# Optimization experiments

Measured on AMD Instinct MI355X. Metric: run time of the kernel, lower is better.

The kernel has to match this reference:

```python
import jax, jax.numpy as jnp
import numpy as np

NEG_SLOPE = 0.2


def _add_self_loops(edge_index, n_nodes):
    loops = jnp.arange(n_nodes, dtype=edge_index.dtype)
    src = jnp.concatenate([edge_index[0], loops])
    dst = jnp.concatenate([edge_index[1], loops])
    return src, dst


def gat_conv(x, src, dst, W, a_src, a_dst, b, n_nodes):
    # h: [N, F] transformed node features
    h = x @ W
    # per-node attention logits, then gather per-edge
    s_n = h @ a_src  # [N]
    d_n = h @ a_dst  # [N]
    e = jax.nn.leaky_relu(s_n[src] + d_n[dst], NEG_SLOPE)  # [E]
    # softmax over incoming edges of each destination node (self-loops guarantee >=1 edge per node)
    m = jax.ops.segment_max(e, dst, num_segments=n_nodes)  # [N]
    p = jnp.exp(e - m[dst])
    denom = jax.ops.segment_sum(p, dst, num_segments=n_nodes)  # [N]
    alpha = p / denom[dst]  # [E]
    # scatter weighted source features to destinations
    out = jax.ops.segment_sum(alpha[:, None] * h[src], dst, num_segments=n_nodes)
    return out + b


def setup_inputs() -> dict:
    key = jax.random.key(0)
    ks = jax.random.split(key, 11)
    N, E, D = 50000, 800000, 128
    x = jax.random.normal(ks[0], (N, D), dtype=jnp.float32)
    edge_index = jax.random.randint(ks[1], (2, E), 0, N, dtype=jnp.int64)
    p = lambda k, shape: jax.random.normal(k, shape, dtype=jnp.float32) * 0.05
    return {
        "x": x,
        "edge_index": edge_index,
        "W1": p(ks[2], (D, D)), "a_src1": p(ks[3], (D,)), "a_dst1": p(ks[4], (D,)), "b1": p(ks[5], (D,)),
        "W2": p(ks[6], (D, D)), "a_src2": p(ks[7], (D,)), "a_dst2": p(ks[8], (D,)), "b2": p(ks[9], (D,)),
    }


def reference(x, edge_index, W1, a_src1, a_dst1, b1, W2, a_src2, a_dst2, b2):
    n_nodes = x.shape[0]
    src, dst = _add_self_loops(edge_index, n_nodes)
    h = jax.nn.relu(gat_conv(x, src, dst, W1, a_src1, a_dst1, b1, n_nodes))
    h = gat_conv(h, src, dst, W2, a_src2, a_dst2, b2, n_nodes)
    return h.mean(axis=0)  # [out_dim]
```

## Files before the change

### kernel.cpp

```cpp
#include <hip/hip_runtime.h>
#include <hip/hip_fp8.h>
#include <math.h>

#define NEG_SLOPE 0.2f
#define D 128
#define SCAN_NB 128
#define NBLK_BIN 256
#define NPB 128
#define LOG_NPB 7

typedef unsigned int uint;
typedef unsigned short ushort;
typedef unsigned char uchar;
typedef short bf16x8 __attribute__((ext_vector_type(8)));
typedef float f32x4 __attribute__((ext_vector_type(4)));

__device__ __forceinline__ float bflo(uint u) { return __uint_as_float(u << 16); }
__device__ __forceinline__ float bfhi(uint u) { return __uint_as_float(u & 0xffff0000u); }
__device__ __forceinline__ uint packbf(float lo, float hi) {
    uint a = __float_as_uint(lo), b = __float_as_uint(hi);
    uint ra = (a + 0x7fffu + ((a >> 16) & 1u)) >> 16;
    uint rb = (b + 0x7fffu + ((b >> 16) & 1u)) >> 16;
    return ra | (rb << 16);
}
__device__ __forceinline__ ushort bf16_1(float f) {
    uint a = __float_as_uint(f);
    return (ushort)((a + 0x7fffu + ((a >> 16) & 1u)) >> 16);
}
__device__ __forceinline__ uint relu_pk(uint u) {
    uint lo = (u & 0x00008000u) ? 0u : (u & 0x0000ffffu);
    uint hi = (u & 0x80000000u) ? 0u : (u & 0xffff0000u);
    return lo | hi;
}

__device__ __forceinline__ float fp8tof(uint b) {
    __hip_fp8_e4m3 v; v.__x = (__hip_fp8_storage_t)b; return (float)v;
}
__device__ __forceinline__ uchar ftofp8(float f) {
    __hip_fp8_e4m3 v(f); return (uchar)v.__x;
}

union U4B { uint4 u; bf16x8 h; };


__global__ __launch_bounds__(256) void bin_hist(const int* __restrict__ dst,
                                                int E, int M, int nbuck,
                                                int* __restrict__ hist) {
    extern __shared__ int lh[];
    for (int k = threadIdx.x; k < nbuck; k += 256) lh[k] = 0;
    __syncthreads();
    int chunk = (M + gridDim.x - 1) / gridDim.x;
    int e0 = blockIdx.x * chunk;
    int e1 = e0 + chunk; if (e1 > M) e1 = M;
    for (int e = e0 + threadIdx.x; e < e1; e += 256) {
        int d = (e < E) ? dst[e] : (e - E);
        atomicAdd(&lh[d >> LOG_NPB], 1);
    }
    __syncthreads();
    for (int k = threadIdx.x; k < nbuck; k += 256)
        hist[(size_t)k * NBLK_BIN + blockIdx.x] = lh[k];
}

__global__ __launch_bounds__(256) void scan_pass1(const int* __restrict__ cnt, int n,
                                                  int* __restrict__ bsum) {
    int chunk = (n + SCAN_NB - 1) / SCAN_NB;
    int b0 = blockIdx.x * chunk;
    int b1 = b0 + chunk; if (b1 > n) b1 = n;
    int s = 0;
    for (int i = b0 + threadIdx.x; i < b1; i += 256) s += cnt[i];
    for (int off = 32; off; off >>= 1) s += __shfl_xor(s, off);
    __shared__ int ws[4];
    int lane = threadIdx.x & 63, wave = threadIdx.x >> 6;
    if (lane == 0) ws[wave] = s;
    __syncthreads();
    if (threadIdx.x == 0) bsum[blockIdx.x] = ws[0] + ws[1] + ws[2] + ws[3];
}

__global__ __launch_bounds__(128) void scan_pass2(int* __restrict__ bsum) {
    int t = threadIdx.x;
    int v = bsum[t];
    int lane = t & 63, wave = t >> 6;
    int x = v;
#pragma unroll
    for (int off = 1; off < 64; off <<= 1) {
        int y = __shfl_up(x, off);
        if (lane >= off) x += y;
    }
    __shared__ int wtot[2];
    if (lane == 63) wtot[wave] = x;
    __syncthreads();
    int base = (wave == 1) ? wtot[0] : 0;
    bsum[t] = base + x - v;
}

__global__ __launch_bounds__(256) void scan_pass3(const int* __restrict__ cnt, int n,
                                                  const int* __restrict__ bsum,
                                                  int* __restrict__ outp, int total) {
    int chunk = (n + SCAN_NB - 1) / SCAN_NB;
    int b0 = blockIdx.x * chunk;
    int b1 = b0 + chunk; if (b1 > n) b1 = n;
    int tchunk = (chunk + 255) / 256;
    int t0 = b0 + threadIdx.x * tchunk;
    int t1 = t0 + tchunk; if (t1 > b1) t1 = b1;
    int s = 0;
    for (int i = t0; i < t1; ++i) s += cnt[i];
    int lane = threadIdx.x & 63, wave = threadIdx.x >> 6;
    int x = s;
#pragma unroll
    for (int off = 1; off < 64; off <<= 1) {
        int y = __shfl_up(x, off);
        if (lane >= off) x += y;
    }
    __shared__ int wtot[4];
    if (lane == 63) wtot[wave] = x;
    __syncthreads();
    int wbase = 0;
    for (int w = 0; w < wave; ++w) wbase += wtot[w];
    int run = bsum[blockIdx.x] + wbase + x - s;
    for (int i = t0; i < t1; ++i) {
        outp[i] = run;
        run += cnt[i];
    }
    if (blockIdx.x == 0 && threadIdx.x == 0) outp[n] = total;
}

__global__ __launch_bounds__(256) void bin_scatter(const int* __restrict__ esrc,
                                                   const int* __restrict__ dst,
                                                   int E, int M, int nbuck,
                                                   const int* __restrict__ hist_off,
                                                   int* __restrict__ packed) {
    extern __shared__ int cur[];
    for (int k = threadIdx.x; k < nbuck; k += 256)
        cur[k] = hist_off[(size_t)k * NBLK_BIN + blockIdx.x];
    __syncthreads();
    int chunk = (M + gridDim.x - 1) / gridDim.x;
    int e0 = blockIdx.x * chunk;
    int e1 = e0 + chunk; if (e1 > M) e1 = M;
    for (int e = e0 + threadIdx.x; e < e1; e += 256) {
        int d, s;
        if (e < E) { d = dst[e]; s = esrc[e]; }
        else       { d = e - E;  s = d; }
        int k = d >> LOG_NPB;
        int pos = atomicAdd(&cur[k], 1);
        packed[pos] = ((d & (NPB - 1)) << 16) | s;
    }
}

__global__ __launch_bounds__(256) void bucket_sort(const int* __restrict__ packed,
                                                   const int* __restrict__ hist_off,
                                                   int N, int M,
                                                   int* __restrict__ row_ptr,
                                                   int* __restrict__ csr_src) {
    __shared__ int lcnt[NPB];
    __shared__ int lcur[NPB];
    __shared__ int wtot2[2];
    int t = threadIdx.x;
    int node0 = blockIdx.x << LOG_NPB;
    int nlocal = N - node0; if (nlocal > NPB) nlocal = NPB;
    int base = hist_off[(size_t)blockIdx.x * NBLK_BIN];
    int bend = hist_off[(size_t)(blockIdx.x + 1) * NBLK_BIN];

    if (t < NPB) lcnt[t] = 0;
    __syncthreads();
    for (int j = base + t; j < bend; j += 256)
        atomicAdd(&lcnt[packed[j] >> 16], 1);
    __syncthreads();

    int v = (t < NPB) ? lcnt[t] : 0;
    int lane = t & 63, wv = t >> 6;
    int x = v;
#pragma unroll
    for (int off = 1; off < 64; off <<= 1) {
        int y = __shfl_up(x, off);
        if (lane >= off) x += y;
    }
    if (t < NPB && lane == 63) wtot2[wv] = x;
    __syncthreads();
    if (t < NPB) {
        int bw = (wv == 1) ? wtot2[0] : 0;
        int ex = bw + x - v;
        lcur[t] = ex;
        if (t < nlocal) row_ptr[node0 + t] = base + ex;
    }
    if (blockIdx.x == 0 && t == 0) row_ptr[N] = M;
    __syncthreads();

    for (int j = base + t; j < bend; j += 256) {
        int p = packed[j];
        int dl = p >> 16;
        int pos = atomicAdd(&lcur[dl], 1);
        csr_src[base + pos] = p & 0xffff;
    }
}

__global__ __launch_bounds__(128) void wt_kernel2(const float* __restrict__ W1,
                                                  const float* __restrict__ W2,
                                                  ushort* __restrict__ Wt1,
                                                  ushort* __restrict__ Wt2) {
    int col = blockIdx.x & 127;
    const float* W = (blockIdx.x < 128) ? W1 : W2;
    ushort* Wt = (blockIdx.x < 128) ? Wt1 : Wt2;
    Wt[(size_t)col * D + threadIdx.x] = bf16_1(W[(size_t)threadIdx.x * D + col]);
}

template <bool RELU_IN, bool BF16_IN>
__global__ __launch_bounds__(256) void gemm_mfma(const void* __restrict__ Xv,
                                                 const ushort* __restrict__ Wt,
                                                 const float* __restrict__ a_src,
                                                 const float* __restrict__ a_dst,
                                                 uchar* __restrict__ H,
                                                 float* __restrict__ s_n,
                                                 float* __restrict__ d_n, int n) {
    __shared__ float sred[2][32][5];
    int wave = threadIdx.x >> 6;
    int lane = threadIdx.x & 63;
    int row0 = blockIdx.x * 32;
    int kgrp = (lane >> 4) * 8;

    bf16x8 afrag[2][4];
#pragma unroll
    for (int rh = 0; rh < 2; ++rh) {
        int arow = row0 + rh * 16 + (lane & 15);
        bool rvalid = arow < n;
        if (BF16_IN) {
            const ushort* X = (const ushort*)Xv;
            const ushort* xp = X + (size_t)arow * D + kgrp;
#pragma unroll
            for (int kk = 0; kk < 4; ++kk) {
                U4B u; u.u = make_uint4(0, 0, 0, 0);
                if (rvalid) {
                    u.u = *(const uint4*)(xp + kk * 32);
                    if (RELU_IN) {
                        u.u.x = relu_pk(u.u.x); u.u.y = relu_pk(u.u.y);
                        u.u.z = relu_pk(u.u.z); u.u.w = relu_pk(u.u.w);
                    }
                }
                afrag[rh][kk] = u.h;
            }
        } else {
            const float* X = (const float*)Xv;
            const float* xp = X + (size_t)arow * D + kgrp;
#pragma unroll
            for (int kk = 0; kk < 4; ++kk) {
                U4B u; u.u = make_uint4(0, 0, 0, 0);
                if (rvalid) {
                    float4 v0 = *(const float4*)(xp + kk * 32);
                    float4 v1 = *(const float4*)(xp + kk * 32 + 4);
                    if (RELU_IN) {
                        v0.x = fmaxf(v0.x, 0.f); v0.y = fmaxf(v0.y, 0.f);
                        v0.z = fmaxf(v0.z, 0.f); v0.w = fmaxf(v0.w, 0.f);
                        v1.x = fmaxf(v1.x, 0.f); v1.y = fmaxf(v1.y, 0.f);
                        v1.z = fmaxf(v1.z, 0.f); v1.w = fmaxf(v1.w, 0.f);
                    }
                    u.u.x = packbf(v0.x, v0.y); u.u.y = packbf(v0.z, v0.w);
                    u.u.z = packbf(v1.x, v1.y); u.u.w = packbf(v1.z, v1.w);
                }
                afrag[rh][kk] = u.h;
            }
        }
    }

    bf16x8 bfrag[2][4];
#pragma unroll
    for (int t = 0; t < 2; ++t) {
        int bcol = wave * 32 + t * 16 + (lane & 15);
        const ushort* wp = Wt + (size_t)bcol * D + kgrp;
#pragma unroll
        for (int kk = 0; kk < 4; ++kk) {
            U4B u; u.u = *(const uint4*)(wp + kk * 32);
            bfrag[t][kk] = u.h;
        }
    }

    f32x4 acc[2][2];
#pragma unroll
    for (int rh = 0; rh < 2; ++rh)
#pragma unroll
        for (int t = 0; t < 2; ++t) acc[rh][t] = (f32x4){0.f, 0.f, 0.f, 0.f};

#pragma unroll
    for (int kk = 0; kk < 4; ++kk) {
#pragma unroll
        for (int rh = 0; rh < 2; ++rh) {
#pragma unroll
            for (int t = 0; t < 2; ++t) {
                acc[rh][t] = __builtin_amdgcn_mfma_f32_16x16x32_bf16(
                    afrag[rh][kk], bfrag[t][kk], acc[rh][t], 0, 0, 0);
            }
        }
    }

    int ccol = wave * 32 + (lane & 15);
    float as0 = a_src[ccol], as1 = a_src[ccol + 16];
    float ad0 = a_dst[ccol], ad1 = a_dst[ccol + 16];
#pragma unroll
    for (int rh = 0; rh < 2; ++rh) {
        int crow0 = row0 + rh * 16 + (lane >> 4) * 4;
#pragma unroll
        for (int i = 0; i < 4; ++i) {
            int r = crow0 + i;
            if (r < n) {
                H[(size_t)r * D + ccol]      = ftofp8(acc[rh][0][i]);
                H[(size_t)r * D + ccol + 16] = ftofp8(acc[rh][1][i]);
            }
            float ps = acc[rh][0][i] * as0 + acc[rh][1][i] * as1;
            float pd = acc[rh][0][i] * ad0 + acc[rh][1][i] * ad1;
#pragma unroll
            for (int off = 1; off < 16; off <<= 1) {
                ps += __shfl_xor(ps, off);
                pd += __shfl_xor(pd, off);
            }
            if ((lane & 15) == 0) {
                int rl = rh * 16 + (lane >> 4) * 4 + i;
                sred[0][rl][wave] = ps;
                sred[1][rl][wave] = pd;
            }
        }
    }
    __syncthreads();
    if (threadIdx.x < 64) {
        int which = threadIdx.x >> 5;
        int rl = threadIdx.x & 31;
        float v = sred[which][rl][0] + sred[which][rl][1] +
                  sred[which][rl][2] + sred[which][rl][3];
        int r = row0 + rl;
        if (r < n) { if (which) d_n[r] = v; else s_n[r] = v; }
    }
}

__global__ __launch_bounds__(256) void gat_aggregate(const uchar* __restrict__ H,
                                                     const float* __restrict__ s_n,
                                                     const float* __restrict__ d_n,
                                                     const int* __restrict__ row_ptr,
                                                     const int* __restrict__ csr_src,
                                                     const float* __restrict__ bias,
                                                     ushort* __restrict__ OUT, int n) {
    __shared__ float lp[4][64];
    __shared__ int   ls[4][64];
    int wave = threadIdx.x >> 6;
    int lane = threadIdx.x & 63;
    int node = blockIdx.x * 4 + wave;
    bool valid = node < n;

    int beg = 0, end = 0;
    float dn = 0.f;
    if (valid) {
        beg = row_ptr[node];
        end = row_ptr[node + 1];
        dn  = d_n[node];
    }
    int deg = end - beg;
    bool small = (deg <= 64);

    int g  = lane >> 4;
    int gl = lane & 15;
    int c0 = gl * 8;

    float p = 0.f;
    int   sidx = 0;
    float inv = 1.0f;

    if (small) {
        float e = -INFINITY;
        if (lane < deg) {
            sidx = csr_src[beg + lane];
            float t = s_n[sidx] + dn;
            e = t > 0.f ? t : NEG_SLOPE * t;
        }
        float m = e;
        for (int off = 32; off; off >>= 1) m = fmaxf(m, __shfl_xor(m, off));
        p = (lane < deg) ? __expf(e - m) : 0.f;
        float sum = p;
        for (int off = 32; off; off >>= 1) sum += __shfl_xor(sum, off);
        inv = 1.0f / sum;
    }
    lp[wave][lane] = p;
    ls[wave][lane] = sidx;
    __syncthreads();
    if (!valid) return;

    float acc[8] = {0.f, 0.f, 0.f, 0.f, 0.f, 0.f, 0.f, 0.f};

    if (small) {
        for (int j = g; j < deg; j += 4) {
            int   sv = ls[wave][j];
            float al = lp[wave][j];
            uint2 hv = *(const uint2*)(H + (size_t)sv * D + c0);
            acc[0] = fmaf(al, fp8tof(hv.x & 0xff), acc[0]);
            acc[1] = fmaf(al, fp8tof((hv.x >> 8) & 0xff), acc[1]);
            acc[2] = fmaf(al, fp8tof((hv.x >> 16) & 0xff), acc[2]);
            acc[3] = fmaf(al, fp8tof(hv.x >> 24), acc[3]);
            acc[4] = fmaf(al, fp8tof(hv.y & 0xff), acc[4]);
            acc[5] = fmaf(al, fp8tof((hv.y >> 8) & 0xff), acc[5]);
            acc[6] = fmaf(al, fp8tof((hv.y >> 16) & 0xff), acc[6]);
            acc[7] = fmaf(al, fp8tof(hv.y >> 24), acc[7]);
        }
    } else {
        float m = -INFINITY;
        for (int j = beg + lane; j < end; j += 64) {
            float t = s_n[csr_src[j]] + dn;
            t = t > 0.f ? t : NEG_SLOPE * t;
            m = fmaxf(m, t);
        }
        for (int off = 32; off; off >>= 1) m = fmaxf(m, __shfl_xor(m, off));
        float sum = 0.f;
        for (int j = beg + lane; j < end; j += 64) {
            float t = s_n[csr_src[j]] + dn;
            t = t > 0.f ? t : NEG_SLOPE * t;
            sum += __expf(t - m);
        }
        for (int off = 32; off; off >>= 1) sum += __shfl_xor(sum, off);
        inv = 1.0f / sum;

        for (int j = beg + g; j < end; j += 4) {
            int s = csr_src[j];
            float t = s_n[s] + dn;
            t = t > 0.f ? t : NEG_SLOPE * t;
            float alpha = __expf(t - m);
            uint2 hv = *(const uint2*)(H + (size_t)s * D + c0);
            acc[0] = fmaf(alpha, fp8tof(hv.x & 0xff), acc[0]);
            acc[1] = fmaf(alpha, fp8tof((hv.x >> 8) & 0xff), acc[1]);
            acc[2] = fmaf(alpha, fp8tof((hv.x >> 16) & 0xff), acc[2]);
            acc[3] = fmaf(alpha, fp8tof(hv.x >> 24), acc[3]);
            acc[4] = fmaf(alpha, fp8tof(hv.y & 0xff), acc[4]);
            acc[5] = fmaf(alpha, fp8tof((hv.y >> 8) & 0xff), acc[5]);
            acc[6] = fmaf(alpha, fp8tof((hv.y >> 16) & 0xff), acc[6]);
            acc[7] = fmaf(alpha, fp8tof(hv.y >> 24), acc[7]);
        }
    }

#pragma unroll
    for (int i = 0; i < 8; ++i) {
        acc[i] += __shfl_xor(acc[i], 16);
        acc[i] += __shfl_xor(acc[i], 32);
    }
    if (g == 0) {
        float4 b0 = *(const float4*)(bias + c0);
        float4 b1 = *(const float4*)(bias + c0 + 4);
        uint4 o;
        o.x = packbf(acc[0] * inv + b0.x, acc[1] * inv + b0.y);
        o.y = packbf(acc[2] * inv + b0.z, acc[3] * inv + b0.w);
        o.z = packbf(acc[4] * inv + b1.x, acc[5] * inv + b1.y);
        o.w = packbf(acc[6] * inv + b1.z, acc[7] * inv + b1.w);
        *(uint4*)(OUT + (size_t)node * D + c0) = o;
    }
}


__global__ void zero_out(float* __restrict__ out) { out[threadIdx.x] = 0.f; }

__global__ __launch_bounds__(256) void mean_reduce(const ushort* __restrict__ X, int n,
                                                   float* __restrict__ out) {
    __shared__ float sacc[16][128];
    int rg = threadIdx.x >> 4;
    int ft = threadIdx.x & 15;
    int c0 = ft * 8;
    float a[8] = {0.f, 0.f, 0.f, 0.f, 0.f, 0.f, 0.f, 0.f};
    int stride = gridDim.x * 16;
    for (int r = blockIdx.x * 16 + rg; r < n; r += stride) {
        uint4 v = *(const uint4*)(X + (size_t)r * D + c0);
        a[0] += bflo(v.x); a[1] += bfhi(v.x);
        a[2] += bflo(v.y); a[3] += bfhi(v.y);
        a[4] += bflo(v.z); a[5] += bfhi(v.z);
        a[6] += bflo(v.w); a[7] += bfhi(v.w);
    }
#pragma unroll
    for (int j = 0; j < 8; ++j) sacc[rg][c0 + j] = a[j];
    __syncthreads();
    if (threadIdx.x < 128) {
        float s = 0.f;
#pragma unroll
        for (int g = 0; g < 16; ++g) s += sacc[g][threadIdx.x];
        atomicAdd(&out[threadIdx.x], s * (1.0f / (float)n));
    }
}


extern "C" void kernel_launch(void* const* d_in, const int* in_sizes, int n_in,
                              void* d_out, int out_size, void* d_ws, size_t ws_size,
                              hipStream_t stream) {
    const float* x      = (const float*)d_in[0];
    const int*   ei     = (const int*)d_in[1];
    const float* W1     = (const float*)d_in[2];
    const float* a_src1 = (const float*)d_in[3];
    const float* a_dst1 = (const float*)d_in[4];
    const float* b1     = (const float*)d_in[5];
    const float* W2     = (const float*)d_in[6];
    const float* a_src2 = (const float*)d_in[7];
    const float* a_dst2 = (const float*)d_in[8];
    const float* b2     = (const float*)d_in[9];
    float* out = (float*)d_out;

    int N = in_sizes[0] / D;
    int E = in_sizes[1] / 2;
    const int* esrc = ei;
    const int* edst = ei + E;
    int M = E + N;
    int NBUCK = (N + NPB - 1) >> LOG_NPB;
    int NHIST = NBUCK * NBLK_BIN;
    size_t smem = (size_t)NBUCK * 4;

    char* p = (char*)d_ws;
    auto alloc = [&](size_t bytes) -> void* {
        void* r = (void*)p;
        p += (bytes + 511) & ~(size_t)511;
        return r;
    };
    int*    hist     = (int*)alloc((size_t)NHIST * 4);
    int*    hist_off = (int*)alloc((size_t)(NHIST + 1) * 4);
    int*    packed   = (int*)alloc((size_t)M * 4);
    int*    csr_src  = (int*)alloc((size_t)M * 4);
    int*    row_ptr  = (int*)alloc((size_t)(N + 1) * 4);
    int*    bsum     = (int*)alloc((size_t)SCAN_NB * 4);
    uchar*  h        = (uchar*)alloc((size_t)N * D);
    ushort* io       = (ushort*)alloc((size_t)N * D * 2);
    float*  s_n      = (float*)alloc((size_t)N * 4);
    float*  d_n      = (float*)alloc((size_t)N * 4);
    ushort* wt1      = (ushort*)alloc((size_t)D * D * 2);
    ushort* wt2      = (ushort*)alloc((size_t)D * D * 2);

    bin_hist<<<NBLK_BIN, 256, smem, stream>>>(edst, E, M, NBUCK, hist);
    scan_pass1<<<SCAN_NB, 256, 0, stream>>>(hist, NHIST, bsum);
    scan_pass2<<<1, 128, 0, stream>>>(bsum);
    scan_pass3<<<SCAN_NB, 256, 0, stream>>>(hist, NHIST, bsum, hist_off, M);
    bin_scatter<<<NBLK_BIN, 256, smem, stream>>>(esrc, edst, E, M, NBUCK, hist_off, packed);
    bucket_sort<<<NBUCK, 256, 0, stream>>>(packed, hist_off, N, M, row_ptr, csr_src);

    wt_kernel2<<<256, 128, 0, stream>>>(W1, W2, wt1, wt2);

    gemm_mfma<false, false><<<(N + 31) / 32, 256, 0, stream>>>(x, wt1, a_src1, a_dst1, h, s_n, d_n, N);
    gat_aggregate<<<(N + 3) / 4, 256, 0, stream>>>(h, s_n, d_n, row_ptr, csr_src, b1, io, N);

    gemm_mfma<true, true><<<(N + 31) / 32, 256, 0, stream>>>(io, wt2, a_src2, a_dst2, h, s_n, d_n, N);
    gat_aggregate<<<(N + 3) / 4, 256, 0, stream>>>(h, s_n, d_n, row_ptr, csr_src, b2, io, N);

    zero_out<<<1, 128, 0, stream>>>(out);
    mean_reduce<<<256, 256, 0, stream>>>(io, N, out);
}
```

Measured before the change: 170.9 us.

## Fuse final mean reduction into second GAT aggregation kernel

The second-layer aggregation is templated so that its FINAL variant accumulates each node's normalized output into per-block partial sums in registers and shared memory, instead of writing a bf16 N×128 tensor. A small final_mean kernel reduces these partials with atomics, and the output is pre-initialized with the bias, since mean(x+b) = mean(x)+b. This removes the full output write plus the separate mean_reduce pass that read it back. In exchange, the final aggregation becomes a grid-stride loop over a fixed 2048 blocks, which may change load balance and occupancy, and it drops the per-iteration __syncthreads around the shared staging buffers.

```diff
diff --git a/kernel.cpp b/kernel.cpp
--- a/kernel.cpp
+++ b/kernel.cpp
@@ -8,6 +8,7 @@
 #define NBLK_BIN 256
 #define NPB 128
 #define LOG_NPB 7
+#define NAGG 2048
 
 typedef unsigned int uint;
 typedef unsigned short ushort;
@@ -328,151 +329,172 @@
     }
 }
 
+template <bool FINAL>
 __global__ __launch_bounds__(256) void gat_aggregate(const uchar* __restrict__ H,
                                                      const float* __restrict__ s_n,
                                                      const float* __restrict__ d_n,
                                                      const int* __restrict__ row_ptr,
                                                      const int* __restrict__ csr_src,
                                                      const float* __restrict__ bias,
-                                                     ushort* __restrict__ OUT, int n) {
+                                                     ushort* __restrict__ OUT,
+                                                     float* __restrict__ partial,
+                                                     int n) {
     __shared__ float lp[4][64];
     __shared__ int   ls[4][64];
+    __shared__ float sacc[4][128];
     int wave = threadIdx.x >> 6;
     int lane = threadIdx.x & 63;
-    int node = blockIdx.x * 4 + wave;
-    bool valid = node < n;
-
-    int beg = 0, end = 0;
-    float dn = 0.f;
-    if (valid) {
-        beg = row_ptr[node];
-        end = row_ptr[node + 1];
-        dn  = d_n[node];
-    }
-    int deg = end - beg;
-    bool small = (deg <= 64);
-
     int g  = lane >> 4;
     int gl = lane & 15;
     int c0 = gl * 8;
 
-    float p = 0.f;
-    int   sidx = 0;
-    float inv = 1.0f;
-
-    if (small) {
-        float e = -INFINITY;
-        if (lane < deg) {
-            sidx = csr_src[beg + lane];
-            float t = s_n[sidx] + dn;
-            e = t > 0.f ? t : NEG_SLOPE * t;
-        }
-        float m = e;
-        for (int off = 32; off; off >>= 1) m = fmaxf(m, __shfl_xor(m, off));
-        p = (lane < deg) ? __expf(e - m) : 0.f;
-        float sum = p;
-        for (int off = 32; off; off >>= 1) sum += __shfl_xor(sum, off);
-        inv = 1.0f / sum;
-    }
-    lp[wave][lane] = p;
-    ls[wave][lane] = sidx;
-    __syncthreads();
-    if (!valid) return;
-
-    float acc[8] = {0.f, 0.f, 0.f, 0.f, 0.f, 0.f, 0.f, 0.f};
-
-    if (small) {
-        for (int j = g; j < deg; j += 4) {
-            int   sv = ls[wave][j];
-            float al = lp[wave][j];
-            uint2 hv = *(const uint2*)(H + (size_t)sv * D + c0);
-            acc[0] = fmaf(al, fp8tof(hv.x & 0xff), acc[0]);
-            acc[1] = fmaf(al, fp8tof((hv.x >> 8) & 0xff), acc[1]);
-            acc[2] = fmaf(al, fp8tof((hv.x >> 16) & 0xff), acc[2]);
-            acc[3] = fmaf(al, fp8tof(hv.x >> 24), acc[3]);
-            acc[4] = fmaf(al, fp8tof(hv.y & 0xff), acc[4]);
-            acc[5] = fmaf(al, fp8tof((hv.y >> 8) & 0xff), acc[5]);
-            acc[6] = fmaf(al, fp8tof((hv.y >> 16) & 0xff), acc[6]);
-            acc[7] = fmaf(al, fp8tof(hv.y >> 24), acc[7]);
-        }
-    } else {
-        float m = -INFINITY;
-        for (int j = beg + lane; j < end; j += 64) {
-            float t = s_n[csr_src[j]] + dn;
-            t = t > 0.f ? t : NEG_SLOPE * t;
-            m = fmaxf(m, t);
-        }
-        for (int off = 32; off; off >>= 1) m = fmaxf(m, __shfl_xor(m, off));
-        float sum = 0.f;
-        for (int j = beg + lane; j < end; j += 64) {
-            float t = s_n[csr_src[j]] + dn;
-            t = t > 0.f ? t : NEG_SLOPE * t;
-            sum += __expf(t - m);
-        }
-        for (int off = 32; off; off >>= 1) sum += __shfl_xor(sum, off);
-        inv = 1.0f / sum;
-
-        for (int j = beg + g; j < end; j += 4) {
-            int s = csr_src[j];
-            float t = s_n[s] + dn;
-            t = t > 0.f ? t : NEG_SLOPE * t;
-            float alpha = __expf(t - m);
-            uint2 hv = *(const uint2*)(H + (size_t)s * D + c0);
-            acc[0] = fmaf(alpha, fp8tof(hv.x & 0xff), acc[0]);
-            acc[1] = fmaf(alpha, fp8tof((hv.x >> 8) & 0xff), acc[1]);
-            acc[2] = fmaf(alpha, fp8tof((hv.x >> 16) & 0xff), acc[2]);
-            acc[3] = fmaf(alpha, fp8tof(hv.x >> 24), acc[3]);
-            acc[4] = fmaf(alpha, fp8tof(hv.y & 0xff), acc[4]);
-            acc[5] = fmaf(alpha, fp8tof((hv.y >> 8) & 0xff), acc[5]);
-            acc[6] = fmaf(alpha, fp8tof((hv.y >> 16) & 0xff), acc[6]);
-            acc[7] = fmaf(alpha, fp8tof(hv.y >> 24), acc[7]);
-        }
-    }
-
-#pragma unroll
-    for (int i = 0; i < 8; ++i) {
-        acc[i] += __shfl_xor(acc[i], 16);
-        acc[i] += __shfl_xor(acc[i], 32);
-    }
-    if (g == 0) {
-        float4 b0 = *(const float4*)(bias + c0);
-        float4 b1 = *(const float4*)(bias + c0 + 4);
-        uint4 o;
-        o.x = packbf(acc[0] * inv + b0.x, acc[1] * inv + b0.y);
-        o.y = packbf(acc[2] * inv + b0.z, acc[3] * inv + b0.w);
-        o.z = packbf(acc[4] * inv + b1.x, acc[5] * inv + b1.y);
-        o.w = packbf(acc[6] * inv + b1.z, acc[7] * inv + b1.w);
-        *(uint4*)(OUT + (size_t)node * D + c0) = o;
-    }
-}
-
-
-__global__ void zero_out(float* __restrict__ out) { out[threadIdx.x] = 0.f; }
-
-__global__ __launch_bounds__(256) void mean_reduce(const ushort* __restrict__ X, int n,
-                                                   float* __restrict__ out) {
-    __shared__ float sacc[16][128];
-    int rg = threadIdx.x >> 4;
-    int ft = threadIdx.x & 15;
-    int c0 = ft * 8;
-    float a[8] = {0.f, 0.f, 0.f, 0.f, 0.f, 0.f, 0.f, 0.f};
-    int stride = gridDim.x * 16;
-    for (int r = blockIdx.x * 16 + rg; r < n; r += stride) {
-        uint4 v = *(const uint4*)(X + (size_t)r * D + c0);
-        a[0] += bflo(v.x); a[1] += bfhi(v.x);
-        a[2] += bflo(v.y); a[3] += bfhi(v.y);
-        a[4] += bflo(v.z); a[5] += bfhi(v.z);
-        a[6] += bflo(v.w); a[7] += bfhi(v.w);
-    }
-#pragma unroll
-    for (int j = 0; j < 8; ++j) sacc[rg][c0 + j] = a[j];
-    __syncthreads();
-    if (threadIdx.x < 128) {
-        float s = 0.f;
-#pragma unroll
-        for (int g = 0; g < 16; ++g) s += sacc[g][threadIdx.x];
-        atomicAdd(&out[threadIdx.x], s * (1.0f / (float)n));
-    }
+    float macc[8] = {0.f, 0.f, 0.f, 0.f, 0.f, 0.f, 0.f, 0.f};
+    int stride = gridDim.x * 4;
+    int iters = FINAL ? (n + stride - 1) / stride : 1;
+
+    for (int it = 0; it < iters; ++it) {
+        int node = blockIdx.x * 4 + wave + it * stride;
+        bool valid = node < n;
+
+        int beg = 0, end = 0;
+        float dn = 0.f;
+        if (valid) {
+            beg = row_ptr[node];
+            end = row_ptr[node + 1];
+            dn  = d_n[node];
+        }
+        int deg = end - beg;
+        bool small = (deg <= 64);
+
+        float p = 0.f;
+        int   sidx = 0;
+        float inv = 1.0f;
+
+        if (small) {
+            float e = -INFINITY;
+            if (lane < deg) {
+                sidx = csr_src[beg + lane];
+                float t = s_n[sidx] + dn;
+                e = t > 0.f ? t : NEG_SLOPE * t;
+            }
+            float m = e;
+            for (int off = 32; off; off >>= 1) m = fmaxf(m, __shfl_xor(m, off));
+            p = (lane < deg) ? __expf(e - m) : 0.f;
+            float sum = p;
+            for (int off = 32; off; off >>= 1) sum += __shfl_xor(sum, off);
+            inv = 1.0f / sum;
+        }
+        lp[wave][lane] = p;
+        ls[wave][lane] = sidx;
+
+        if (valid) {
+            float acc[8] = {0.f, 0.f, 0.f, 0.f, 0.f, 0.f, 0.f, 0.f};
+
+            if (small) {
+                for (int j = g; j < deg; j += 4) {
+                    int   sv = ls[wave][j];
+                    float al = lp[wave][j];
+                    uint2 hv = *(const uint2*)(H + (size_t)sv * D + c0);
+                    acc[0] = fmaf(al, fp8tof(hv.x & 0xff), acc[0]);
+                    acc[1] = fmaf(al, fp8tof((hv.x >> 8) & 0xff), acc[1]);
+                    acc[2] = fmaf(al, fp8tof((hv.x >> 16) & 0xff), acc[2]);
+                    acc[3] = fmaf(al, fp8tof(hv.x >> 24), acc[3]);
+                    acc[4] = fmaf(al, fp8tof(hv.y & 0xff), acc[4]);
+                    acc[5] = fmaf(al, fp8tof((hv.y >> 8) & 0xff), acc[5]);
+                    acc[6] = fmaf(al, fp8tof((hv.y >> 16) & 0xff), acc[6]);
+                    acc[7] = fmaf(al, fp8tof(hv.y >> 24), acc[7]);
+                }
+            } else {
+                float m = -INFINITY;
+                for (int j = beg + lane; j < end; j += 64) {
+                    float t = s_n[csr_src[j]] + dn;
+                    t = t > 0.f ? t : NEG_SLOPE * t;
+                    m = fmaxf(m, t);
+                }
+                for (int off = 32; off; off >>= 1) m = fmaxf(m, __shfl_xor(m, off));
+                float sum = 0.f;
+                for (int j = beg + lane; j < end; j += 64) {
+                    float t = s_n[csr_src[j]] + dn;
+                    t = t > 0.f ? t : NEG_SLOPE * t;
+                    sum += __expf(t - m);
+                }
+                for (int off = 32; off; off >>= 1) sum += __shfl_xor(sum, off);
+                inv = 1.0f / sum;
+
+                for (int j = beg + g; j < end; j += 4) {
+                    int s = csr_src[j];
+                    float t = s_n[s] + dn;
+                    t = t > 0.f ? t : NEG_SLOPE * t;
+                    float alpha = __expf(t - m);
+                    uint2 hv = *(const uint2*)(H + (size_t)s * D + c0);
+                    acc[0] = fmaf(alpha, fp8tof(hv.x & 0xff), acc[0]);
+                    acc[1] = fmaf(alpha, fp8tof((hv.x >> 8) & 0xff), acc[1]);
+                    acc[2] = fmaf(alpha, fp8tof((hv.x >> 16) & 0xff), acc[2]);
+                    acc[3] = fmaf(alpha, fp8tof(hv.x >> 24), acc[3]);
+                    acc[4] = fmaf(alpha, fp8tof(hv.y & 0xff), acc[4]);
+                    acc[5] = fmaf(alpha, fp8tof((hv.y >> 8) & 0xff), acc[5]);
+                    acc[6] = fmaf(alpha, fp8tof((hv.y >> 16) & 0xff), acc[6]);
+                    acc[7] = fmaf(alpha, fp8tof(hv.y >> 24), acc[7]);
+                }
+            }
+
+#pragma unroll
+            for (int i = 0; i < 8; ++i) {
+                acc[i] += __shfl_xor(acc[i], 16);
+                acc[i] += __shfl_xor(acc[i], 32);
+            }
+            if (g == 0) {
+                if (FINAL) {
+#pragma unroll
+                    for (int i = 0; i < 8; ++i) macc[i] += acc[i] * inv;
+                } else {
+                    float4 b0 = *(const float4*)(bias + c0);
+                    float4 b1 = *(const float4*)(bias + c0 + 4);
+                    uint4 o;
+                    o.x = packbf(acc[0] * inv + b0.x, acc[1] * inv + b0.y);
+                    o.y = packbf(acc[2] * inv + b0.z, acc[3] * inv + b0.w);
+                    o.z = packbf(acc[4] * inv + b1.x, acc[5] * inv + b1.y);
+                    o.w = packbf(acc[6] * inv + b1.z, acc[7] * inv + b1.w);
+                    *(uint4*)(OUT + (size_t)node * D + c0) = o;
+                }
+            }
+        }
+    }
+
+    if (FINAL) {
+        if (g == 0) {
+#pragma unroll
+            for (int i = 0; i < 8; ++i) sacc[wave][c0 + i] = macc[i];
+        }
+        __syncthreads();
+        if (threadIdx.x < 128) {
+            float s = sacc[0][threadIdx.x] + sacc[1][threadIdx.x] +
+                      sacc[2][threadIdx.x] + sacc[3][threadIdx.x];
+            partial[(size_t)blockIdx.x * 128 + threadIdx.x] = s;
+        }
+    }
+}
+
+
+__global__ void init_out(const float* __restrict__ b, float* __restrict__ out) {
+    out[threadIdx.x] = b[threadIdx.x];
+}
+
+__global__ __launch_bounds__(256) void final_mean(const float* __restrict__ partial,
+                                                  int nblk, float inv_n,
+                                                  float* __restrict__ out) {
+    __shared__ float red[2][128];
+    int f = threadIdx.x & 127;
+    int hh = threadIdx.x >> 7;
+    int r0 = blockIdx.x * 128;
+    int r1 = r0 + 128; if (r1 > nblk) r1 = nblk;
+    float s = 0.f;
+    for (int r = r0 + hh; r < r1; r += 2)
+        s += partial[(size_t)r * 128 + f];
+    red[hh][f] = s;
+    __syncthreads();
+    if (threadIdx.x < 128)
+        atomicAdd(&out[f], (red[0][f] + red[1][f]) * inv_n);
 }
 
 
@@ -518,6 +540,7 @@
     float*  d_n      = (float*)alloc((size_t)N * 4);
     ushort* wt1      = (ushort*)alloc((size_t)D * D * 2);
     ushort* wt2      = (ushort*)alloc((size_t)D * D * 2);
+    float*  partial  = (float*)alloc((size_t)NAGG * 128 * 4);
 
     bin_hist<<<NBLK_BIN, 256, smem, stream>>>(edst, E, M, NBUCK, hist);
     scan_pass1<<<SCAN_NB, 256, 0, stream>>>(hist, NHIST, bsum);
@@ -529,11 +552,10 @@
     wt_kernel2<<<256, 128, 0, stream>>>(W1, W2, wt1, wt2);
 
     gemm_mfma<false, false><<<(N + 31) / 32, 256, 0, stream>>>(x, wt1, a_src1, a_dst1, h, s_n, d_n, N);
-    gat_aggregate<<<(N + 3) / 4, 256, 0, stream>>>(h, s_n, d_n, row_ptr, csr_src, b1, io, N);
+    gat_aggregate<false><<<(N + 3) / 4, 256, 0, stream>>>(h, s_n, d_n, row_ptr, csr_src, b1, io, nullptr, N);
 
     gemm_mfma<true, true><<<(N + 31) / 32, 256, 0, stream>>>(io, wt2, a_src2, a_dst2, h, s_n, d_n, N);
-    gat_aggregate<<<(N + 3) / 4, 256, 0, stream>>>(h, s_n, d_n, row_ptr, csr_src, b2, io, N);
-
-    zero_out<<<1, 128, 0, stream>>>(out);
-    mean_reduce<<<256, 256, 0, stream>>>(io, N, out);
-}
+    init_out<<<1, 128, 0, stream>>>(b2, out);
+    gat_aggregate<true><<<NAGG, 256, 0, stream>>>(h, s_n, d_n, row_ptr, csr_src, b2, nullptr, partial, N);
+    final_mean<<<(NAGG + 127) / 128, 256, 0, stream>>>(partial, NAGG, 1.0f / (float)N, out);
+}
```

Result: no change. 172.8 us (+1.1%).
